# Kernel optimization log

Measured on AMD Instinct MI355X. Metric: run time of the kernel, lower is better.

The kernel has to match this reference:

```python
import jax, jax.numpy as jnp
import numpy as np
import math

WINDOW_SIZE = 1024
CAUSAL = True


def setup_inputs() -> dict:
    key = jax.random.key(0)
    kq, kk, kv = jax.random.split(key, 3)
    B, H, L, D = 2, 16, 4096, 128
    q = jax.random.normal(kq, (B, H, L, D), dtype=jnp.float32)
    k = jax.random.normal(kk, (B, H, L, D), dtype=jnp.float32)
    v = jax.random.normal(kv, (B, H, L, D), dtype=jnp.float32)
    return {"q": q, "k": k, "v": v}


def _sliding_window_attention(q, k, v):
    # Faithful port of SlidingWindowAttention._blockwise_attention (L > 2048 path).
    B, H, L, D = q.shape
    block = min(WINDOW_SIZE, 1024)
    scale = 1.0 / math.sqrt(D)
    half_w = WINDOW_SIZE // 2
    outs = []
    # Python loop over a small fixed number of blocks (L/block = 4), not data dims.
    for s in range(0, L, block):
        e = min(s + block, L)
        ks = max(0, s - half_w)
        ke = min(L, e + half_w)
        if CAUSAL:
            ke = min(ke, e)
        qb = q[:, :, s:e, :]          # [B,H,Q,D]
        kb = k[:, :, ks:ke, :]        # [B,H,K,D]
        vb = v[:, :, ks:ke, :]        # [B,H,K,D]
        scores = jnp.einsum('bhqd,bhkd->bhqk', qb, kb) * scale
        if CAUSAL:
            qi = jnp.arange(s, e)[:, None]   # [Q,1]
            ki = jnp.arange(ks, ke)[None, :]  # [1,K]
            causal_mask = qi >= ki            # [Q,K]
            scores = jnp.where(causal_mask[None, None], scores, -jnp.inf)
        attn = jax.nn.softmax(scores, axis=-1)
        outs.append(jnp.einsum('bhqk,bhkd->bhqd', attn, vb))
    return jnp.concatenate(outs, axis=2)


def reference(q, k, v):
    return _sliding_window_attention(q, k, v)
```

## Files before the change

### kernel.cpp

```cpp
#include <hip/hip_runtime.h>
#include <hip/hip_bf16.h>
#include <stdint.h>

typedef __bf16 bf16_t;
typedef __bf16 bf16x8 __attribute__((ext_vector_type(8)));
typedef __bf16 bf16x4 __attribute__((ext_vector_type(4)));
typedef float f32x4 __attribute__((ext_vector_type(4)));

#define L_SEQ 4096
#define D_DIM 128
#define NBH   32
#define KT    32

__global__ __launch_bounds__(256)
void cvt_k(const float* __restrict__ Kg, bf16_t* __restrict__ Kws) {
    const int n   = blockIdx.x * 256 + threadIdx.x;
    const int key = n >> 4;
    const int pc  = n & 15;
    const int lc  = pc ^ (key & 7);
    const float* s = Kg + (size_t)key * D_DIM + lc * 8;
    f32x4 a = *(const f32x4*)(s);
    f32x4 b = *(const f32x4*)(s + 4);
    bf16x8 h;
    #pragma unroll
    for (int j = 0; j < 4; ++j) { h[j] = (bf16_t)a[j]; h[4 + j] = (bf16_t)b[j]; }
    *(bf16x8*)(Kws + (size_t)key * D_DIM + pc * 8) = h;
}

__global__ __launch_bounds__(256)
void cvt_v(const float* __restrict__ Vg, bf16_t* __restrict__ Vws) {
    const int blk  = blockIdx.x;
    const int bh   = blk >> 7;
    const int kb   = blk & 127;
    const int t    = threadIdx.x;
    const int d    = t & 127;
    const int half = t >> 7;
    const float* src0 = Vg + (size_t)(bh * L_SEQ + kb * 32) * D_DIM + d;
    bf16_t* dstrow = Vws + ((size_t)(bh * 128 + kb) * D_DIM + d) * 32;
    const int sw = (d >> 1) & 3;
    #pragma unroll
    for (int r2 = 0; r2 < 2; ++r2) {
        const int lc = half + 2 * r2;
        bf16x8 h;
        #pragma unroll
        for (int j = 0; j < 8; ++j)
            h[j] = (bf16_t)src0[(size_t)(lc * 8 + j) * D_DIM];
        *(bf16x8*)(&dstrow[(lc ^ sw) * 8]) = h;
    }
}

__device__ __forceinline__ void ld_lds16(const void* g, void* s) {
    __builtin_amdgcn_global_load_lds(
        (const __attribute__((address_space(1))) unsigned int*)g,
        (__attribute__((address_space(3))) unsigned int*)s, 16, 0, 0);
}

#define QT2 128

__global__ __launch_bounds__(256, 3)
void swa_fwd3(const float* __restrict__ Qg,
              const bf16_t* __restrict__ Kws,
              const bf16_t* __restrict__ Vws,
              float* __restrict__ Og) {
    __shared__ __align__(16) bf16_t KtS[2][KT * D_DIM];
    __shared__ __align__(16) bf16_t VtS[2][D_DIM * KT];
    __shared__ __align__(16) bf16_t Pst[4][16 * KT];

    const int t    = threadIdx.x;
    const int w    = t >> 6;
    const int ln   = t & 15;
    const int quad = (t & 63) >> 4;
    const int l7   = t & 7;

    const int id = blockIdx.x;
    const int bh = id & 31;
    const int g  = id >> 5;
    const int r_ = g & 7;
    const int k_ = g >> 3;
    const int qt = 8 * k_ + ((k_ & 1) ? (7 - r_) : r_);

    const size_t baseF = (size_t)bh * L_SEQ * D_DIM;
    const float*  Qp = Qg + baseF;
    float*        Op = Og + baseF;
    const bf16_t* Kb = Kws + baseF;
    const bf16_t* Vb = Vws + (size_t)bh * 128 * D_DIM * 32;

    const int qbase  = qt * QT2;
    const int blk    = qbase & ~1023;
    const int kstart = (blk - 512) > 0 ? (blk - 512) : 0;
    const int kend   = qbase + QT2;
    const int ntile  = (kend - kstart) / KT;

    const int qw    = qbase + w * 32;
    const int qwmax = qw + 31;

    const float SC  = 0.08838834764831845f * 1.4426950408889634f;
    const float FIX = 8.0f;
    const float NEG = -1.0e30f;

    bf16x8 qf[2][4];
    #pragma unroll
    for (int mt = 0; mt < 2; ++mt) {
        const float* qrow = Qp + (size_t)(qw + mt * 16 + ln) * D_DIM + quad * 8;
        #pragma unroll
        for (int ks = 0; ks < 4; ++ks) {
            f32x4 a = *(const f32x4*)(qrow + ks * 32);
            f32x4 b = *(const f32x4*)(qrow + ks * 32 + 4);
            bf16x8 q8;
            #pragma unroll
            for (int j = 0; j < 4; ++j) { q8[j] = (bf16_t)(a[j] * SC); q8[4 + j] = (bf16_t)(b[j] * SC); }
            qf[mt][ks] = q8;
        }
    }

    f32x4 Oacc[2][8];
    #pragma unroll
    for (int mt = 0; mt < 2; ++mt)
        #pragma unroll
        for (int dt = 0; dt < 8; ++dt) Oacc[mt][dt] = f32x4{0.f, 0.f, 0.f, 0.f};
    float lsum[2] = {0.f, 0.f};

    auto stage = [&](int b, int k0) {
        const char* ksrc = (const char*)Kb + (size_t)k0 * 256;
        const char* vsrc = (const char*)Vb + (size_t)(k0 >> 5) * 8192;
        char* kd = (char*)(&KtS[b][0]);
        char* vd = (char*)(&VtS[b][0]);
        #pragma unroll
        for (int i = 0; i < 2; ++i) {
            const int off = (i * 256 + t) * 16;
            ld_lds16(ksrc + off, kd + off);
            ld_lds16(vsrc + off, vd + off);
        }
    };

    stage(0, kstart);
    __syncthreads();

    int buf = 0;
    for (int kt = 0; kt < ntile; ++kt) {
        const int k0 = kstart + kt * KT;
        if (kt + 1 < ntile) stage(buf ^ 1, k0 + KT);

        if (k0 <= qwmax) {
            f32x4 S[2][2];
            #pragma unroll
            for (int mt = 0; mt < 2; ++mt)
                #pragma unroll
                for (int nt = 0; nt < 2; ++nt) S[mt][nt] = f32x4{0.f, 0.f, 0.f, 0.f};
            __builtin_amdgcn_s_setprio(1);
            #pragma unroll
            for (int ks = 0; ks < 4; ++ks) {
                #pragma unroll
                for (int nt = 0; nt < 2; ++nt) {
                    const bf16x8 bk = *(const bf16x8*)(
                        &KtS[buf][(nt * 16 + ln) * D_DIM + (((ks * 4 + quad) ^ l7) * 8)]);
                    S[0][nt] = __builtin_amdgcn_mfma_f32_16x16x32_bf16(bk, qf[0][ks], S[0][nt], 0, 0, 0);
                    S[1][nt] = __builtin_amdgcn_mfma_f32_16x16x32_bf16(bk, qf[1][ks], S[1][nt], 0, 0, 0);
                }
            }
            __builtin_amdgcn_s_setprio(0);

            bf16x8 pa[2];
            #pragma unroll
            for (int mt = 0; mt < 2; ++mt) {
                const int qwm = qw + mt * 16;
                const int qg  = qwm + ln;
                const bool nm = (k0 + KT - 1) > qwm;
                #pragma unroll
                for (int nt = 0; nt < 2; ++nt) {
                    bf16x4 hp;
                    #pragma unroll
                    for (int r = 0; r < 4; ++r) {
                        float s = S[mt][nt][r];
                        if (nm) {
                            const int kg = k0 + nt * 16 + quad * 4 + r;
                            if (kg > qg) s = NEG;
                        }
                        const float e = __builtin_amdgcn_exp2f(s - FIX);
                        lsum[mt] += e;
                        hp[r] = (bf16_t)e;
                    }
                    *(bf16x4*)(&Pst[w][ln * KT +
                        (((nt * 2 + (quad >> 1)) ^ (ln & 3)) * 8) + (quad & 1) * 4]) = hp;
                }
                pa[mt] = *(const bf16x8*)(&Pst[w][ln * KT + ((quad ^ (ln & 3)) * 8)]);
            }

            __builtin_amdgcn_s_setprio(1);
            #pragma unroll
            for (int dt = 0; dt < 8; ++dt) {
                const bf16x8 bv = *(const bf16x8*)(
                    &VtS[buf][(dt * 16 + ln) * KT + ((quad ^ ((ln >> 1) & 3)) * 8)]);
                Oacc[0][dt] = __builtin_amdgcn_mfma_f32_16x16x32_bf16(bv, pa[0], Oacc[0][dt], 0, 0, 0);
                Oacc[1][dt] = __builtin_amdgcn_mfma_f32_16x16x32_bf16(bv, pa[1], Oacc[1][dt], 0, 0, 0);
            }
            __builtin_amdgcn_s_setprio(0);
        }

        __syncthreads();
        buf ^= 1;
    }

    #pragma unroll
    for (int mt = 0; mt < 2; ++mt) {
        float l = lsum[mt];
        l += __shfl_xor(l, 16, 64);
        l += __shfl_xor(l, 32, 64);
        const float inv = (l > 0.f) ? (1.f / l) : 0.f;
        const int qg = qw + mt * 16 + ln;
        float* orow = Op + (size_t)qg * D_DIM + quad * 4;
        #pragma unroll
        for (int dt = 0; dt < 8; ++dt) {
            f32x4 o = Oacc[mt][dt];
            #pragma unroll
            for (int j = 0; j < 4; ++j) o[j] *= inv;
            *(f32x4*)(orow + dt * 16) = o;
        }
    }
}

#define QTF 64
#define KTF 64
#define LDK 136
#define LDV 72
#define LDP 72

__global__ __launch_bounds__(256, 2)
void swa_fwd(const float* __restrict__ Qg,
             const float* __restrict__ Kg,
             const float* __restrict__ Vg,
             float* __restrict__ Og) {
    __shared__ __align__(16) bf16_t Kt[KTF][LDK];
    __shared__ __align__(16) bf16_t Vt[D_DIM][LDV];
    __shared__ __align__(16) bf16_t Pstf[4][16][LDP];

    const int t    = threadIdx.x;
    const int w    = t >> 6;
    const int ln   = t & 15;
    const int quad = (t & 63) >> 4;

    const int id = blockIdx.x;
    const int bh = id & 31;
    const int g  = id >> 5;
    const int q0 = g & 7;
    const int kk = g >> 3;
    const int qt = 16 * (kk >> 1) + ((kk & 1) ? (15 - q0) : q0);

    const size_t base = (size_t)bh * L_SEQ * D_DIM;
    const float* Qp = Qg + base;
    const float* Kp = Kg + base;
    const float* Vp = Vg + base;
    float*       Op = Og + base;

    const int qbase  = qt * QTF;
    const int blk    = qbase & ~1023;
    const int kstart = (blk - 512) > 0 ? (blk - 512) : 0;
    const int kend   = qbase + QTF;
    const int ntile  = (kend - kstart) / KTF;

    const int qw = qbase + w * 16;

    const float SC  = 0.08838834764831845f * 1.4426950408889634f;
    const float FIX = 8.0f;

    bf16x8 qf[4];
    {
        const float* qrow = Qp + (size_t)(qw + ln) * D_DIM + quad * 8;
        #pragma unroll
        for (int ks = 0; ks < 4; ++ks) {
            f32x4 a = *(const f32x4*)(qrow + ks * 32);
            f32x4 b = *(const f32x4*)(qrow + ks * 32 + 4);
            bf16x8 q8;
            #pragma unroll
            for (int j = 0; j < 4; ++j) {
                q8[j]     = (bf16_t)(a[j] * SC);
                q8[4 + j] = (bf16_t)(b[j] * SC);
            }
            qf[ks] = q8;
        }
    }

    f32x4 Oacc[8];
    #pragma unroll
    for (int dt = 0; dt < 8; ++dt) Oacc[dt] = f32x4{0.f, 0.f, 0.f, 0.f};
    float lsum[4] = {0.f, 0.f, 0.f, 0.f};
    const float NEG = -1.0e30f;

    const int kr   = t >> 5;
    const int kc   = t & 31;
    const int vd   = t & 127;
    const int vkcb = t >> 7;

    f32x4 kreg[8];
    float vreg[4][8];

    auto load_tile = [&](int k0) {
        #pragma unroll
        for (int i = 0; i < 8; ++i)
            kreg[i] = *(const f32x4*)(Kp + (size_t)(k0 + kr + 8 * i) * D_DIM + kc * 4);
        #pragma unroll
        for (int r2 = 0; r2 < 4; ++r2) {
            const int kcc = vkcb + 2 * r2;
            #pragma unroll
            for (int j = 0; j < 8; ++j)
                vreg[r2][j] = Vp[(size_t)(k0 + kcc * 8 + j) * D_DIM + vd];
        }
    };
    auto store_tile = [&]() {
        #pragma unroll
        for (int i = 0; i < 8; ++i) {
            bf16x4 h;
            #pragma unroll
            for (int j = 0; j < 4; ++j) h[j] = (bf16_t)kreg[i][j];
            *(bf16x4*)(&Kt[kr + 8 * i][kc * 4]) = h;
        }
        #pragma unroll
        for (int r2 = 0; r2 < 4; ++r2) {
            const int kcc = vkcb + 2 * r2;
            bf16x8 h8;
            #pragma unroll
            for (int j = 0; j < 8; ++j) h8[j] = (bf16_t)vreg[r2][j];
            *(bf16x8*)(&Vt[vd][kcc * 8]) = h8;
        }
    };

    load_tile(kstart);

    for (int kt = 0; kt < ntile; ++kt) {
        const int k0 = kstart + kt * KTF;
        __syncthreads();
        store_tile();
        __syncthreads();
        if (kt + 1 < ntile) load_tile(k0 + KTF);

        f32x4 S[4];
        #pragma unroll
        for (int nt = 0; nt < 4; ++nt) S[nt] = f32x4{0.f, 0.f, 0.f, 0.f};
        #pragma unroll
        for (int ks = 0; ks < 4; ++ks) {
            #pragma unroll
            for (int nt = 0; nt < 4; ++nt) {
                bf16x8 bk = *(const bf16x8*)(&Kt[nt * 16 + ln][quad * 8 + ks * 32]);
                S[nt] = __builtin_amdgcn_mfma_f32_16x16x32_bf16(qf[ks], bk, S[nt], 0, 0, 0);
            }
        }

        const bool lastTile = (kt == ntile - 1);
        float p[4][4];
        #pragma unroll
        for (int nt = 0; nt < 4; ++nt) {
            #pragma unroll
            for (int r = 0; r < 4; ++r) {
                float s = S[nt][r];
                if (lastTile) {
                    const int kg = k0 + nt * 16 + ln;
                    const int qg = qw + quad * 4 + r;
                    if (kg > qg) s = NEG;
                }
                const float e = __builtin_amdgcn_exp2f(s - FIX);
                p[nt][r] = e;
                lsum[r] += e;
            }
        }

        #pragma unroll
        for (int nt = 0; nt < 4; ++nt)
            #pragma unroll
            for (int r = 0; r < 4; ++r)
                Pstf[w][quad * 4 + r][nt * 16 + ln] = (bf16_t)p[nt][r];

        bf16x8 pa[2];
        #pragma unroll
        for (int ks2 = 0; ks2 < 2; ++ks2)
            pa[ks2] = *(const bf16x8*)(&Pstf[w][ln][quad * 8 + ks2 * 32]);

        #pragma unroll
        for (int dt = 0; dt < 8; ++dt) {
            #pragma unroll
            for (int ks2 = 0; ks2 < 2; ++ks2) {
                bf16x8 bv = *(const bf16x8*)(&Vt[dt * 16 + ln][quad * 8 + ks2 * 32]);
                Oacc[dt] = __builtin_amdgcn_mfma_f32_16x16x32_bf16(pa[ks2], bv, Oacc[dt], 0, 0, 0);
            }
        }
    }

    #pragma unroll
    for (int r = 0; r < 4; ++r) {
        float l = lsum[r];
        #pragma unroll
        for (int msk = 1; msk < 16; msk <<= 1)
            l += __shfl_xor(l, msk, 64);
        const float inv = (l > 0.f) ? (1.f / l) : 0.f;
        const int qg = qw + quad * 4 + r;
        float* orow = Op + (size_t)qg * D_DIM + ln;
        #pragma unroll
        for (int dt = 0; dt < 8; ++dt)
            orow[dt * 16] = Oacc[dt][r] * inv;
    }
}

extern "C" void kernel_launch(void* const* d_in, const int* in_sizes, int n_in,
                              void* d_out, int out_size, void* d_ws, size_t ws_size,
                              hipStream_t stream) {
    const float* q = (const float*)d_in[0];
    const float* k = (const float*)d_in[1];
    const float* v = (const float*)d_in[2];
    float* o = (float*)d_out;

    const size_t kbytes = (size_t)NBH * L_SEQ * D_DIM * sizeof(bf16_t);
    if (d_ws && ws_size >= 2 * kbytes) {
        bf16_t* kws = (bf16_t*)d_ws;
        bf16_t* vws = (bf16_t*)((char*)d_ws + kbytes);
        cvt_k<<<dim3(8192), dim3(256), 0, stream>>>(k, kws);
        cvt_v<<<dim3(4096), dim3(256), 0, stream>>>(v, vws);
        swa_fwd3<<<dim3(1024), dim3(256), 0, stream>>>(q, kws, vws, o);
    } else {
        swa_fwd<<<dim3(2048), dim3(256), 0, stream>>>(q, k, v, o);
    }
}
```

Baseline: 305.5 us.

## Triple-buffer K/V staging with vmcnt waits and merge conversion kernels

The attention kernel moves from double to triple buffering of K/V tiles in LDS. It prefetches two tiles ahead and replaces the full __syncthreads with explicit vmcnt waits plus s_barrier, which should hide more global-load latency. The K and V bf16 conversion kernels are merged into one launch to cut launch overhead. The P staging buffer switches from an XOR swizzle to a padded stride. The extra LDS buffer raises shared memory per block and may lower occupancy below the 3-blocks bound.

```diff
diff --git a/kernel.cpp b/kernel.cpp
--- a/kernel.cpp
+++ b/kernel.cpp
@@ -11,41 +11,43 @@
 #define D_DIM 128
 #define NBH   32
 #define KT    32
+#define LDP   36
 
 __global__ __launch_bounds__(256)
-void cvt_k(const float* __restrict__ Kg, bf16_t* __restrict__ Kws) {
-    const int n   = blockIdx.x * 256 + threadIdx.x;
-    const int key = n >> 4;
-    const int pc  = n & 15;
-    const int lc  = pc ^ (key & 7);
-    const float* s = Kg + (size_t)key * D_DIM + lc * 8;
-    f32x4 a = *(const f32x4*)(s);
-    f32x4 b = *(const f32x4*)(s + 4);
-    bf16x8 h;
-    #pragma unroll
-    for (int j = 0; j < 4; ++j) { h[j] = (bf16_t)a[j]; h[4 + j] = (bf16_t)b[j]; }
-    *(bf16x8*)(Kws + (size_t)key * D_DIM + pc * 8) = h;
-}
-
-__global__ __launch_bounds__(256)
-void cvt_v(const float* __restrict__ Vg, bf16_t* __restrict__ Vws) {
-    const int blk  = blockIdx.x;
-    const int bh   = blk >> 7;
-    const int kb   = blk & 127;
-    const int t    = threadIdx.x;
-    const int d    = t & 127;
-    const int half = t >> 7;
-    const float* src0 = Vg + (size_t)(bh * L_SEQ + kb * 32) * D_DIM + d;
-    bf16_t* dstrow = Vws + ((size_t)(bh * 128 + kb) * D_DIM + d) * 32;
-    const int sw = (d >> 1) & 3;
-    #pragma unroll
-    for (int r2 = 0; r2 < 2; ++r2) {
-        const int lc = half + 2 * r2;
+void cvt_kv(const float* __restrict__ Kg, const float* __restrict__ Vg,
+            bf16_t* __restrict__ Kws, bf16_t* __restrict__ Vws) {
+    const int b = blockIdx.x;
+    if (b < 8192) {
+        const int n   = b * 256 + threadIdx.x;
+        const int key = n >> 4;
+        const int pc  = n & 15;
+        const int lc  = pc ^ (key & 7);
+        const float* s = Kg + (size_t)key * D_DIM + lc * 8;
+        f32x4 a = *(const f32x4*)(s);
+        f32x4 c = *(const f32x4*)(s + 4);
         bf16x8 h;
         #pragma unroll
-        for (int j = 0; j < 8; ++j)
-            h[j] = (bf16_t)src0[(size_t)(lc * 8 + j) * D_DIM];
-        *(bf16x8*)(&dstrow[(lc ^ sw) * 8]) = h;
+        for (int j = 0; j < 4; ++j) { h[j] = (bf16_t)a[j]; h[4 + j] = (bf16_t)c[j]; }
+        *(bf16x8*)(Kws + (size_t)key * D_DIM + pc * 8) = h;
+    } else {
+        const int blk  = b - 8192;
+        const int bh   = blk >> 7;
+        const int kb   = blk & 127;
+        const int t    = threadIdx.x;
+        const int d    = t & 127;
+        const int half = t >> 7;
+        const float* src0 = Vg + (size_t)(bh * L_SEQ + kb * 32) * D_DIM + d;
+        bf16_t* dstrow = Vws + ((size_t)(bh * 128 + kb) * D_DIM + d) * 32;
+        const int sw = (d >> 1) & 3;
+        #pragma unroll
+        for (int r2 = 0; r2 < 2; ++r2) {
+            const int lc = half + 2 * r2;
+            bf16x8 h;
+            #pragma unroll
+            for (int j = 0; j < 8; ++j)
+                h[j] = (bf16_t)src0[(size_t)(lc * 8 + j) * D_DIM];
+            *(bf16x8*)(&dstrow[(lc ^ sw) * 8]) = h;
+        }
     }
 }
 
@@ -58,13 +60,13 @@
 #define QT2 128
 
 __global__ __launch_bounds__(256, 3)
-void swa_fwd3(const float* __restrict__ Qg,
+void swa_fwd4(const float* __restrict__ Qg,
               const bf16_t* __restrict__ Kws,
               const bf16_t* __restrict__ Vws,
               float* __restrict__ Og) {
-    __shared__ __align__(16) bf16_t KtS[2][KT * D_DIM];
-    __shared__ __align__(16) bf16_t VtS[2][D_DIM * KT];
-    __shared__ __align__(16) bf16_t Pst[4][16 * KT];
+    __shared__ __align__(16) bf16_t KtS[3][KT * D_DIM];
+    __shared__ __align__(16) bf16_t VtS[3][D_DIM * KT];
+    __shared__ __align__(16) bf16_t Pst[4][16 * LDP];
 
     const int t    = threadIdx.x;
     const int w    = t >> 6;
@@ -120,26 +122,29 @@
         for (int dt = 0; dt < 8; ++dt) Oacc[mt][dt] = f32x4{0.f, 0.f, 0.f, 0.f};
     float lsum[2] = {0.f, 0.f};
 
-    auto stage = [&](int b, int k0) {
+    auto stage = [&](bf16_t* kd_, bf16_t* vd_, int k0) {
         const char* ksrc = (const char*)Kb + (size_t)k0 * 256;
         const char* vsrc = (const char*)Vb + (size_t)(k0 >> 5) * 8192;
-        char* kd = (char*)(&KtS[b][0]);
-        char* vd = (char*)(&VtS[b][0]);
         #pragma unroll
         for (int i = 0; i < 2; ++i) {
             const int off = (i * 256 + t) * 16;
-            ld_lds16(ksrc + off, kd + off);
-            ld_lds16(vsrc + off, vd + off);
+            ld_lds16(ksrc + off, (char*)kd_ + off);
+            ld_lds16(vsrc + off, (char*)vd_ + off);
         }
     };
 
-    stage(0, kstart);
-    __syncthreads();
-
-    int buf = 0;
-    for (int kt = 0; kt < ntile; ++kt) {
-        const int k0 = kstart + kt * KT;
-        if (kt + 1 < ntile) stage(buf ^ 1, k0 + KT);
+    bf16_t *kc = &KtS[0][0], *kn = &KtS[1][0], *kf = &KtS[2][0];
+    bf16_t *vc = &VtS[0][0], *vn = &VtS[1][0], *vf = &VtS[2][0];
+
+    stage(kc, vc, kstart);
+    stage(kn, vn, kstart + KT);
+    asm volatile("s_waitcnt vmcnt(4)" ::: "memory");
+    __builtin_amdgcn_s_barrier();
+    __builtin_amdgcn_sched_barrier(0);
+
+    for (int n = 0; n < ntile; ++n) {
+        const int k0 = kstart + n * KT;
+        if (n + 2 < ntile) stage(kf, vf, k0 + 2 * KT);
 
         if (k0 <= qwmax) {
             f32x4 S[2][2];
@@ -153,7 +158,7 @@
                 #pragma unroll
                 for (int nt = 0; nt < 2; ++nt) {
                     const bf16x8 bk = *(const bf16x8*)(
-                        &KtS[buf][(nt * 16 + ln) * D_DIM + (((ks * 4 + quad) ^ l7) * 8)]);
+                        &kc[(nt * 16 + ln) * D_DIM + (((ks * 4 + quad) ^ l7) * 8)]);
                     S[0][nt] = __builtin_amdgcn_mfma_f32_16x16x32_bf16(bk, qf[0][ks], S[0][nt], 0, 0, 0);
                     S[1][nt] = __builtin_amdgcn_mfma_f32_16x16x32_bf16(bk, qf[1][ks], S[1][nt], 0, 0, 0);
                 }
@@ -180,25 +185,34 @@
                         lsum[mt] += e;
                         hp[r] = (bf16_t)e;
                     }
-                    *(bf16x4*)(&Pst[w][ln * KT +
-                        (((nt * 2 + (quad >> 1)) ^ (ln & 3)) * 8) + (quad & 1) * 4]) = hp;
+                    *(bf16x4*)(&Pst[w][ln * LDP + (nt * 2 + (quad >> 1)) * 8 + (quad & 1) * 4]) = hp;
                 }
-                pa[mt] = *(const bf16x8*)(&Pst[w][ln * KT + ((quad ^ (ln & 3)) * 8)]);
+                pa[mt] = *(const bf16x8*)(&Pst[w][ln * LDP + quad * 8]);
             }
 
             __builtin_amdgcn_s_setprio(1);
             #pragma unroll
             for (int dt = 0; dt < 8; ++dt) {
                 const bf16x8 bv = *(const bf16x8*)(
-                    &VtS[buf][(dt * 16 + ln) * KT + ((quad ^ ((ln >> 1) & 3)) * 8)]);
+                    &vc[(dt * 16 + ln) * KT + ((quad ^ ((ln >> 1) & 3)) * 8)]);
                 Oacc[0][dt] = __builtin_amdgcn_mfma_f32_16x16x32_bf16(bv, pa[0], Oacc[0][dt], 0, 0, 0);
                 Oacc[1][dt] = __builtin_amdgcn_mfma_f32_16x16x32_bf16(bv, pa[1], Oacc[1][dt], 0, 0, 0);
             }
             __builtin_amdgcn_s_setprio(0);
         }
 
-        __syncthreads();
-        buf ^= 1;
+        if (n + 1 < ntile) {
+            if (n + 2 < ntile) {
+                asm volatile("s_waitcnt vmcnt(4)" ::: "memory");
+            } else {
+                asm volatile("s_waitcnt vmcnt(0)" ::: "memory");
+            }
+            __builtin_amdgcn_s_barrier();
+            __builtin_amdgcn_sched_barrier(0);
+        }
+
+        bf16_t* tk = kc; kc = kn; kn = kf; kf = tk;
+        bf16_t* tv = vc; vc = vn; vn = vf; vf = tv;
     }
 
     #pragma unroll
@@ -223,7 +237,7 @@
 #define KTF 64
 #define LDK 136
 #define LDV 72
-#define LDP 72
+#define LDPF 72
 
 __global__ __launch_bounds__(256, 2)
 void swa_fwd(const float* __restrict__ Qg,
@@ -232,7 +246,7 @@
              float* __restrict__ Og) {
     __shared__ __align__(16) bf16_t Kt[KTF][LDK];
     __shared__ __align__(16) bf16_t Vt[D_DIM][LDV];
-    __shared__ __align__(16) bf16_t Pstf[4][16][LDP];
+    __shared__ __align__(16) bf16_t Pstf[4][16][LDPF];
 
     const int t    = threadIdx.x;
     const int w    = t >> 6;
@@ -411,9 +425,8 @@
     if (d_ws && ws_size >= 2 * kbytes) {
         bf16_t* kws = (bf16_t*)d_ws;
         bf16_t* vws = (bf16_t*)((char*)d_ws + kbytes);
-        cvt_k<<<dim3(8192), dim3(256), 0, stream>>>(k, kws);
-        cvt_v<<<dim3(4096), dim3(256), 0, stream>>>(v, vws);
-        swa_fwd3<<<dim3(1024), dim3(256), 0, stream>>>(q, kws, vws, o);
+        cvt_kv<<<dim3(12288), dim3(256), 0, stream>>>(k, v, kws, vws);
+        swa_fwd4<<<dim3(1024), dim3(256), 0, stream>>>(q, kws, vws, o);
     } else {
         swa_fwd<<<dim3(2048), dim3(256), 0, stream>>>(q, k, v, o);
     }
```

Result: faster. 279.1 us (-8.6%).
